# Kernel tuning notes

Measured on AMD Instinct MI355X. Metric: run time of the kernel, lower is better.

## Reference

```python
import jax, jax.numpy as jnp
import numpy as np

B, S, C = 4096, 6, 2048  # batch, num_strips, in_channel
D = C // 8               # query/key projection dim

def setup_inputs() -> dict:
    key = jax.random.key(0)
    k1, k2, k3, k4 = jax.random.split(key, 4)
    sc = 1.0 / np.sqrt(C)
    return {
        "x": jax.random.normal(k1, (B, S, C), dtype=jnp.float32),
        "Wq": jax.random.normal(k2, (D, C), dtype=jnp.float32) * sc,
        "Wk": jax.random.normal(k3, (D, C), dtype=jnp.float32) * sc,
        "Wv": jax.random.normal(k4, (C, C), dtype=jnp.float32) * sc,
        "gamma": jnp.ones((1,), dtype=jnp.float32),
    }

def reference(x, Wq, Wk, Wv, gamma):
    # x: [B, S, C] stacked squeezed strips (feat in the torch code)
    q = jnp.einsum('bsc,dc->bsd', x, Wq)          # [B, S, D]
    k = jnp.einsum('bsc,dc->bsd', x, Wk)          # [B, S, D]
    energy = jnp.einsum('bsd,btd->bst', q, k)     # [B, S, S]
    attention = jax.nn.softmax(energy, axis=-1)   # softmax over keys
    v = jnp.einsum('bsc,dc->bsd', x, Wv)          # [B, S, C]
    out = jnp.einsum('bst,btc->bsc', attention, v)  # [B, S, C]
    out = gamma * out + x                         # gamma-scaled residual
    return out, attention
```

## Files before the change

kernel.cpp:

```cpp
#include <hip/hip_runtime.h>

typedef __attribute__((ext_vector_type(4))) float f32x4;
typedef __attribute__((ext_vector_type(8))) _Float16 f16x8;
typedef __attribute__((ext_vector_type(4))) unsigned short u16x4;
typedef __attribute__((ext_vector_type(8))) unsigned short u16x8;

#define NB 4096
#define NS 6
#define NC 2048
#define MTOT (NB * NS)

static __device__ __forceinline__ unsigned short f2h_bits(float f) {
  _Float16 h = (_Float16)f;
  unsigned short b;
  __builtin_memcpy(&b, &h, 2);
  return b;
}
static __device__ __forceinline__ float h2f(unsigned short b) {
  _Float16 h;
  __builtin_memcpy(&h, &b, 2);
  return (float)h;
}

__global__ void split_x_kernel(const float* __restrict__ x,
                               unsigned short* __restrict__ hi,
                               unsigned short* __restrict__ lo, int n4) {
  int i = blockIdx.x * blockDim.x + threadIdx.x;
  const int stride = gridDim.x * blockDim.x;
  for (; i < n4; i += stride) {
    f32x4 v = reinterpret_cast<const f32x4*>(x)[i];
    u16x4 h, l;
#pragma unroll
    for (int j = 0; j < 4; ++j) {
      const unsigned short hb = f2h_bits(v[j]);
      h[j] = hb;
      l[j] = f2h_bits(v[j] - h2f(hb));
    }
    reinterpret_cast<u16x4*>(hi)[i] = h;
    reinterpret_cast<u16x4*>(lo)[i] = l;
  }
}

__global__ void prep_wqk_kernel(const float* __restrict__ Wq,
                                const float* __restrict__ Wk,
                                unsigned short* __restrict__ w) {
  int i = blockIdx.x * blockDim.x + threadIdx.x;
  const int stride = gridDim.x * blockDim.x;
  for (; i < 262144; i += stride) {
    const int row = i >> 9;
    const int col4 = i & 511;
    const float* src = (row < 256) ? (Wq + (size_t)row * NC)
                                   : (Wk + (size_t)(row - 256) * NC);
    f32x4 v = reinterpret_cast<const f32x4*>(src)[col4];
    u16x4 o;
#pragma unroll
    for (int j = 0; j < 4; ++j) o[j] = f2h_bits(v[j]);
    reinterpret_cast<u16x4*>(w)[i] = o;
  }
}

__global__ void conv_f16_kernel(const float* __restrict__ in,
                                unsigned short* __restrict__ out, int n4) {
  int i = blockIdx.x * blockDim.x + threadIdx.x;
  const int stride = gridDim.x * blockDim.x;
  for (; i < n4; i += stride) {
    f32x4 v = reinterpret_cast<const f32x4*>(in)[i];
    u16x4 o;
#pragma unroll
    for (int j = 0; j < 4; ++j) o[j] = f2h_bits(v[j]);
    reinterpret_cast<u16x4*>(out)[i] = o;
  }
}


#define FENCE() asm volatile("" ::: "memory")
#define BAR() do { FENCE(); __builtin_amdgcn_s_barrier(); FENCE(); } while (0)
#define VM4BAR() do { FENCE(); asm volatile("s_waitcnt vmcnt(4)" ::: "memory"); \
                      __builtin_amdgcn_s_barrier(); FENCE(); } while (0)

template <int MB>
__device__ __forceinline__ void mfma_blk(f32x4 (&acc)[8][4], const f16x8 (&Av)[4],
                                         const f16x8 (&Bv)[4]) {
  __builtin_amdgcn_s_setprio(1);
#pragma unroll
  for (int m = 0; m < 4; ++m)
#pragma unroll
    for (int n = 0; n < 4; ++n)
      acc[MB + m][n] =
          __builtin_amdgcn_mfma_f32_16x16x32_f16(Av[m], Bv[n], acc[MB + m][n], 0, 0, 0);
  __builtin_amdgcn_s_setprio(0);
}

__device__ __forceinline__ void load4(f16x8 (&dst)[4], const char* base, int kk) {
#pragma unroll
  for (int m = 0; m < 4; ++m)
    dst[m] = *reinterpret_cast<const f16x8*>(base + (m * 2 + kk) * 1024);
}

__device__ __forceinline__ void stage_op(const unsigned short* g, int row0, int k0,
                                         char* ldsOp, int wid, int lane) {
  const int sl = lane ^ ((lane >> 4) & 1) ^ (((lane >> 5) & 1) << 1);
#pragma unroll
  for (int h = 0; h < 2; ++h)
#pragma unroll
    for (int i = 0; i < 2; ++i) {
      const int c = wid * 2 + i;
      const unsigned short* src =
          g + (size_t)(row0 + h * 128 + (c >> 1) * 16 + (sl >> 2)) * 2048 +
          (unsigned)(k0 + (c & 1) * 32 + (sl & 3) * 8);
      __builtin_amdgcn_global_load_lds(
          (__attribute__((address_space(1))) void*)src,
          (__attribute__((address_space(3))) void*)(ldsOp + h * 16384 + c * 1024),
          16, 0, 0);
    }
}

template <int NSEG, int N, bool EPI, bool NFAST>
__global__ void __launch_bounds__(512, 2)
gemm256(const unsigned short* __restrict__ A0, const unsigned short* __restrict__ B0,
        const unsigned short* __restrict__ A1, const unsigned short* __restrict__ B1,
        const unsigned short* __restrict__ A2, const unsigned short* __restrict__ B2,
        float* __restrict__ C, const float* __restrict__ resid,
        const float* __restrict__ gam) {
  constexpr int NTPS = 2048 / 64;
  constexpr int NT = NSEG * NTPS;
  constexpr int MT = MTOT / 256;
  constexpr int NXT = N / 256;
  constexpr int NWG = MT * NXT;
  constexpr int CPX = NWG / 8;
  __shared__ char lds[131072];

  const int bid = blockIdx.x;
  const int wg = (bid & 7) * CPX + (bid >> 3);
  const int bx = NFAST ? (wg % NXT) : (wg / MT);
  const int by = NFAST ? (wg / NXT) : (wg % MT);
  const int m0 = by * 256, n0 = bx * 256;

  const int t = threadIdx.x;
  const int lane = t & 63;
  const int wid = t >> 6;
  const int wr = wid >> 2, wc = wid & 3;
  const int laneOff = (lane & 15) * 64 + (lane >> 4) * 16;
  const int swzOff = laneOff ^ (((laneOff >> 9) & 1) << 5) ^ (((laneOff >> 8) & 1) << 4);

  f32x4 acc[8][4] = {};
  f16x8 A03[4], A47[4], Bk0[4], Bk1[4];

  const int aBase = wr * 16384 + swzOff;
  const int bBase = 32768 + (wc >> 1) * 16384 + (wc & 1) * 8192 + swzOff;

#define SEL(P0, P1, P2, S) ((NSEG == 1) ? (P0) : ((S) == 0 ? (P0) : ((S) == 1 ? (P1) : (P2))))
#define WRAPT(TT) ((TT) >= NT ? (TT) - NT : (TT))
#define STAGE_A(TT) do { int tw_ = WRAPT(TT); int s_ = tw_ / NTPS; \
    stage_op(SEL(A0, A1, A2, s_), m0, (tw_ % NTPS) * 64, lds + ((TT) & 1) * 65536, wid, lane); } while (0)
#define STAGE_B(TT) do { int tw_ = WRAPT(TT); int s_ = tw_ / NTPS; \
    stage_op(SEL(B0, B1, B2, s_), n0, (tw_ % NTPS) * 64, lds + ((TT) & 1) * 65536 + 32768, wid, lane); } while (0)

  STAGE_A(0);
  STAGE_B(0);
  STAGE_B(1);
  VM4BAR();

#define TILE(TAU, FIRST) do { \
    char* bufc = lds + ((TAU) & 1) * 65536; \
     \
    load4(A03, bufc + aBase, 0); \
    load4(Bk0, bufc + bBase, 0); \
    STAGE_A((TAU) + 1); \
    BAR(); \
    if (!(FIRST)) mfma_blk<4>(acc, A47, Bk1); \
    BAR(); \
     \
    load4(A47, bufc + aBase + 8192, 0); \
    BAR(); \
    mfma_blk<0>(acc, A03, Bk0); \
    BAR(); \
     \
    load4(A03, bufc + aBase, 1); \
    load4(Bk1, bufc + bBase, 1); \
    BAR(); \
    mfma_blk<4>(acc, A47, Bk0); \
    BAR(); \
     \
    load4(A47, bufc + aBase + 8192, 1); \
    STAGE_B((TAU) + 2); \
    VM4BAR(); \
    mfma_blk<0>(acc, A03, Bk1); \
    BAR(); \
  } while (0)

  TILE(0, 1);
  for (int tau = 1; tau < NT; ++tau) TILE(tau, 0);
  mfma_blk<4>(acc, A47, Bk1);

#undef TILE
#undef STAGE_A
#undef STAGE_B
#undef WRAPT
#undef SEL

  const float g = EPI ? gam[0] : 0.f;
#pragma unroll
  for (int m = 0; m < 8; ++m)
#pragma unroll
    for (int n = 0; n < 4; ++n)
#pragma unroll
      for (int j = 0; j < 4; ++j) {
        const int r = m0 + wr * 128 + m * 16 + (lane >> 4) * 4 + j;
        const int c = n0 + wc * 64 + n * 16 + (lane & 15);
        const size_t idx = (size_t)r * (size_t)N + (size_t)c;
        float v = acc[m][n][j];
        if (EPI) v = g * v + resid[idx];
        C[idx] = v;
      }
}

__global__ void __launch_bounds__(256)
attn_fuse(const float* __restrict__ QK,
          const unsigned short* __restrict__ xh,
          float* __restrict__ attn_out,
          unsigned short* __restrict__ y)
{
  __shared__ float qk[NS * 512];
  __shared__ float eng[36];
  __shared__ float att[36];
  const int b = blockIdx.x;
  const int t = threadIdx.x;
  {
    const f32x4* src = reinterpret_cast<const f32x4*>(QK + (size_t)b * (NS * 512));
    f32x4* dst = reinterpret_cast<f32x4*>(qk);
    for (int i = t; i < (NS * 512) / 4; i += 256) dst[i] = src[i];
  }
  __syncthreads();
  if (t < 144) {
    const int s = t / 24;
    const int rem = t - s * 24;
    const int u = rem >> 2;
    const int sub = rem & 3;
    const float* qr = qk + s * 512;
    const float* kr = qk + u * 512 + 256;
    float sum = 0.f;
    const int d0 = sub * 64;
#pragma unroll 4
    for (int d = 0; d < 64; ++d) sum += qr[d0 + d] * kr[d0 + d];
    sum += __shfl_xor(sum, 1);
    sum += __shfl_xor(sum, 2);
    if (sub == 0) eng[s * 6 + u] = sum;
  }
  __syncthreads();
  if (t < 6) {
    float e[6];
#pragma unroll
    for (int u = 0; u < 6; ++u) e[u] = eng[t * 6 + u];
    float mx = e[0];
#pragma unroll
    for (int u = 1; u < 6; ++u) mx = fmaxf(mx, e[u]);
    float p[6];
    float sm = 0.f;
#pragma unroll
    for (int u = 0; u < 6; ++u) { p[u] = expf(e[u] - mx); sm += p[u]; }
    const float inv = 1.0f / sm;
#pragma unroll
    for (int u = 0; u < 6; ++u) {
      const float a = p[u] * inv;
      att[t * 6 + u] = a;
      attn_out[(size_t)b * 36 + t * 6 + u] = a;
    }
  }
  __syncthreads();
  const unsigned short* xb = xh + (size_t)b * (NS * NC);
  unsigned short* yb = y + (size_t)b * (NS * NC);
  const int c0 = t * 8;
  f32x4 xv[12];
#pragma unroll
  for (int u = 0; u < 6; ++u) {
    u16x8 v = *reinterpret_cast<const u16x8*>(xb + u * NC + c0);
#pragma unroll
    for (int j = 0; j < 4; ++j) {
      xv[2 * u][j] = h2f(v[j]);
      xv[2 * u + 1][j] = h2f(v[4 + j]);
    }
  }
#pragma unroll
  for (int s = 0; s < 6; ++s) {
    f32x4 a0 = 0.f, a1 = 0.f;
#pragma unroll
    for (int u = 0; u < 6; ++u) {
      const float w = att[s * 6 + u];
      a0 += w * xv[2 * u];
      a1 += w * xv[2 * u + 1];
    }
    u16x8 o;
#pragma unroll
    for (int j = 0; j < 4; ++j) { o[j] = f2h_bits(a0[j]); o[4 + j] = f2h_bits(a1[j]); }
    *reinterpret_cast<u16x8*>(yb + s * NC + c0) = o;
  }
}

extern "C" void kernel_launch(void* const* d_in, const int* in_sizes, int n_in,
                              void* d_out, int out_size, void* d_ws, size_t ws_size,
                              hipStream_t stream) {
  (void)in_sizes; (void)n_in; (void)out_size; (void)ws_size;
  const float* x   = (const float*)d_in[0];
  const float* Wq  = (const float*)d_in[1];
  const float* Wk  = (const float*)d_in[2];
  const float* Wv  = (const float*)d_in[3];
  const float* gam = (const float*)d_in[4];
  float* out = (float*)d_out;
  float* attn_out = out + (size_t)MTOT * NC;

  char* ws = (char*)d_ws;
  unsigned short* xh  = (unsigned short*)(ws);
  unsigned short* xl  = (unsigned short*)(ws + 100663296ull);
  unsigned short* wqk = (unsigned short*)(ws + 201326592ull);
  unsigned short* wvh = (unsigned short*)(ws + 203423744ull);
  float*          qkb = (float*)(ws + 211812352ull);

  split_x_kernel<<<2048, 256, 0, stream>>>(x, xh, xl, MTOT * NC / 4);
  prep_wqk_kernel<<<256, 256, 0, stream>>>(Wq, Wk, wqk);
  conv_f16_kernel<<<512, 256, 0, stream>>>(Wv, wvh, NC * NC / 4);

  gemm256<2, 512, false, false><<<192, 512, 0, stream>>>(
      xh, wqk, xl, wqk, nullptr, nullptr, qkb, nullptr, nullptr);

  attn_fuse<<<NB, 256, 0, stream>>>(qkb, xh, attn_out, xl);

  gemm256<1, 2048, true, true><<<768, 512, 0, stream>>>(
      xl, wvh, nullptr, nullptr, nullptr, nullptr, out, x, gam);
}
```

Measured before the change: 491.7 us.

## Split QK GEMM hi/lo K-segments across workgroups and deepen LDS pipeline to 4 stages

The QK projection GEMM no longer loops over both hi and lo halves of x in one workgroup. It launches twice as many workgroups, each handling one segment, and writes two partial results that attn_fuse sums when it loads them. This targets the under-filled 192-workgroup launch on the GPU. The GEMM mainloop also moves from a 2-buffer K=64 tile to a 4-buffer K=32 tile ring with a vmcnt(8) wait, so more global loads are in flight. The cost is an extra partial buffer (held temporarily in the output region), extra reads in attn_fuse, and a change to the schedule of the big V GEMM, which may help or hurt it.

```diff
diff --git a/kernel.cpp b/kernel.cpp
--- a/kernel.cpp
+++ b/kernel.cpp
@@ -75,8 +75,7 @@
 
 #define FENCE() asm volatile("" ::: "memory")
 #define BAR() do { FENCE(); __builtin_amdgcn_s_barrier(); FENCE(); } while (0)
-#define VM4BAR() do { FENCE(); asm volatile("s_waitcnt vmcnt(4)" ::: "memory"); \
-                      __builtin_amdgcn_s_barrier(); FENCE(); } while (0)
+#define VM8() do { FENCE(); asm volatile("s_waitcnt vmcnt(8)" ::: "memory"); } while (0)
 
 template <int MB>
 __device__ __forceinline__ void mfma_blk(f32x4 (&acc)[8][4], const f16x8 (&Av)[4],
@@ -91,50 +90,55 @@
   __builtin_amdgcn_s_setprio(0);
 }
 
-__device__ __forceinline__ void load4(f16x8 (&dst)[4], const char* base, int kk) {
+__device__ __forceinline__ void load4(f16x8 (&dst)[4], const char* base) {
 #pragma unroll
   for (int m = 0; m < 4; ++m)
-    dst[m] = *reinterpret_cast<const f16x8*>(base + (m * 2 + kk) * 1024);
-}
-
-__device__ __forceinline__ void stage_op(const unsigned short* g, int row0, int k0,
-                                         char* ldsOp, int wid, int lane) {
+    dst[m] = *reinterpret_cast<const f16x8*>(base + m * 1024);
+}
+
+__device__ __forceinline__ void stage_tile(const unsigned short* gA,
+                                           const unsigned short* gB, int m0, int n0,
+                                           int k0, char* buf, int wid, int lane) {
   const int sl = lane ^ ((lane >> 4) & 1) ^ (((lane >> 5) & 1) << 1);
-#pragma unroll
-  for (int h = 0; h < 2; ++h)
-#pragma unroll
-    for (int i = 0; i < 2; ++i) {
-      const int c = wid * 2 + i;
-      const unsigned short* src =
-          g + (size_t)(row0 + h * 128 + (c >> 1) * 16 + (sl >> 2)) * 2048 +
-          (unsigned)(k0 + (c & 1) * 32 + (sl & 3) * 8);
-      __builtin_amdgcn_global_load_lds(
-          (__attribute__((address_space(1))) void*)src,
-          (__attribute__((address_space(3))) void*)(ldsOp + h * 16384 + c * 1024),
-          16, 0, 0);
-    }
-}
-
-template <int NSEG, int N, bool EPI, bool NFAST>
+  const int rr = sl >> 2;
+  const int kc = (sl & 3) * 8;
+#pragma unroll
+  for (int i = 0; i < 2; ++i) {
+    const int c = wid * 2 + i;
+    const unsigned short* sA = gA + (size_t)(m0 + c * 16 + rr) * 2048 + (k0 + kc);
+    __builtin_amdgcn_global_load_lds(
+        (__attribute__((address_space(1))) void*)sA,
+        (__attribute__((address_space(3))) void*)(buf + c * 1024), 16, 0, 0);
+    const unsigned short* sB = gB + (size_t)(n0 + c * 16 + rr) * 2048 + (k0 + kc);
+    __builtin_amdgcn_global_load_lds(
+        (__attribute__((address_space(1))) void*)sB,
+        (__attribute__((address_space(3))) void*)(buf + 16384 + c * 1024), 16, 0, 0);
+  }
+}
+
+template <int N, bool EPI, bool NFAST, bool SPLIT>
 __global__ void __launch_bounds__(512, 2)
-gemm256(const unsigned short* __restrict__ A0, const unsigned short* __restrict__ B0,
-        const unsigned short* __restrict__ A1, const unsigned short* __restrict__ B1,
-        const unsigned short* __restrict__ A2, const unsigned short* __restrict__ B2,
-        float* __restrict__ C, const float* __restrict__ resid,
+gemm256(const unsigned short* __restrict__ Ahi, const unsigned short* __restrict__ Alo,
+        const unsigned short* __restrict__ B, float* __restrict__ C0,
+        float* __restrict__ C1, const float* __restrict__ resid,
         const float* __restrict__ gam) {
-  constexpr int NTPS = 2048 / 64;
-  constexpr int NT = NSEG * NTPS;
+  constexpr int NT = 64;
   constexpr int MT = MTOT / 256;
   constexpr int NXT = N / 256;
-  constexpr int NWG = MT * NXT;
+  constexpr int NWGb = MT * NXT;
+  constexpr int NWG = SPLIT ? 2 * NWGb : NWGb;
   constexpr int CPX = NWG / 8;
   __shared__ char lds[131072];
 
   const int bid = blockIdx.x;
   const int wg = (bid & 7) * CPX + (bid >> 3);
-  const int bx = NFAST ? (wg % NXT) : (wg / MT);
-  const int by = NFAST ? (wg / NXT) : (wg % MT);
+  const int seg = SPLIT ? (wg >= NWGb ? 1 : 0) : 0;
+  const int w2 = wg - seg * NWGb;
+  const int bx = NFAST ? (w2 % NXT) : (w2 / MT);
+  const int by = NFAST ? (w2 / NXT) : (w2 % MT);
   const int m0 = by * 256, n0 = bx * 256;
+  const unsigned short* A = seg ? Alo : Ahi;
+  float* C = seg ? C1 : C0;
 
   const int t = threadIdx.x;
   const int lane = t & 63;
@@ -142,62 +146,55 @@
   const int wr = wid >> 2, wc = wid & 3;
   const int laneOff = (lane & 15) * 64 + (lane >> 4) * 16;
   const int swzOff = laneOff ^ (((laneOff >> 9) & 1) << 5) ^ (((laneOff >> 8) & 1) << 4);
+  const int aOff = wr * 8192 + swzOff;
+  const int bOff = 16384 + wc * 4096 + swzOff;
 
   f32x4 acc[8][4] = {};
-  f16x8 A03[4], A47[4], Bk0[4], Bk1[4];
-
-  const int aBase = wr * 16384 + swzOff;
-  const int bBase = 32768 + (wc >> 1) * 16384 + (wc & 1) * 8192 + swzOff;
-
-#define SEL(P0, P1, P2, S) ((NSEG == 1) ? (P0) : ((S) == 0 ? (P0) : ((S) == 1 ? (P1) : (P2))))
+  f16x8 A03[4], A47[4], Be[4], Bo[4];
+
 #define WRAPT(TT) ((TT) >= NT ? (TT) - NT : (TT))
-#define STAGE_A(TT) do { int tw_ = WRAPT(TT); int s_ = tw_ / NTPS; \
-    stage_op(SEL(A0, A1, A2, s_), m0, (tw_ % NTPS) * 64, lds + ((TT) & 1) * 65536, wid, lane); } while (0)
-#define STAGE_B(TT) do { int tw_ = WRAPT(TT); int s_ = tw_ / NTPS; \
-    stage_op(SEL(B0, B1, B2, s_), n0, (tw_ % NTPS) * 64, lds + ((TT) & 1) * 65536 + 32768, wid, lane); } while (0)
-
-  STAGE_A(0);
-  STAGE_B(0);
-  STAGE_B(1);
-  VM4BAR();
-
-#define TILE(TAU, FIRST) do { \
-    char* bufc = lds + ((TAU) & 1) * 65536; \
-     \
-    load4(A03, bufc + aBase, 0); \
-    load4(Bk0, bufc + bBase, 0); \
-    STAGE_A((TAU) + 1); \
+#define STAGE(TT) stage_tile(A, B, m0, n0, WRAPT(TT) * 32, lds + ((TT) & 3) * 32768, wid, lane)
+
+  STAGE(0);
+  STAGE(1);
+  STAGE(2);
+  VM8();
+  BAR();
+
+#define PH0(TAU, BREG, DOMF, BPREV) do { \
+    char* bufc = lds + ((TAU) & 3) * 32768; \
+    load4(A03, bufc + aOff); \
+    load4(BREG, bufc + bOff); \
+    STAGE((TAU) + 3); \
     BAR(); \
-    if (!(FIRST)) mfma_blk<4>(acc, A47, Bk1); \
-    BAR(); \
-     \
-    load4(A47, bufc + aBase + 8192, 0); \
-    BAR(); \
-    mfma_blk<0>(acc, A03, Bk0); \
-    BAR(); \
-     \
-    load4(A03, bufc + aBase, 1); \
-    load4(Bk1, bufc + bBase, 1); \
-    BAR(); \
-    mfma_blk<4>(acc, A47, Bk0); \
-    BAR(); \
-     \
-    load4(A47, bufc + aBase + 8192, 1); \
-    STAGE_B((TAU) + 2); \
-    VM4BAR(); \
-    mfma_blk<0>(acc, A03, Bk1); \
+    if (DOMF) mfma_blk<4>(acc, A47, BPREV); \
     BAR(); \
   } while (0)
-
-  TILE(0, 1);
-  for (int tau = 1; tau < NT; ++tau) TILE(tau, 0);
-  mfma_blk<4>(acc, A47, Bk1);
-
-#undef TILE
-#undef STAGE_A
-#undef STAGE_B
+#define PH1(TAU, BREG) do { \
+    char* bufc = lds + ((TAU) & 3) * 32768; \
+    load4(A47, bufc + aOff + 4096); \
+    VM8(); \
+    BAR(); \
+    mfma_blk<0>(acc, A03, BREG); \
+    BAR(); \
+  } while (0)
+
+  PH0(0, Be, false, Bo);
+  PH1(0, Be);
+  PH0(1, Bo, true, Be);
+  PH1(1, Bo);
+  for (int tau = 2; tau < NT; tau += 2) {
+    PH0(tau, Be, true, Bo);
+    PH1(tau, Be);
+    PH0(tau + 1, Bo, true, Be);
+    PH1(tau + 1, Bo);
+  }
+  mfma_blk<4>(acc, A47, Bo);
+
+#undef PH0
+#undef PH1
+#undef STAGE
 #undef WRAPT
-#undef SEL
 
   const float g = EPI ? gam[0] : 0.f;
 #pragma unroll
@@ -216,7 +213,8 @@
 }
 
 __global__ void __launch_bounds__(256)
-attn_fuse(const float* __restrict__ QK,
+attn_fuse(const float* __restrict__ QK1,
+          const float* __restrict__ QK2,
           const unsigned short* __restrict__ xh,
           float* __restrict__ attn_out,
           unsigned short* __restrict__ y)
@@ -227,9 +225,10 @@
   const int b = blockIdx.x;
   const int t = threadIdx.x;
   {
-    const f32x4* src = reinterpret_cast<const f32x4*>(QK + (size_t)b * (NS * 512));
+    const f32x4* s1 = reinterpret_cast<const f32x4*>(QK1 + (size_t)b * (NS * 512));
+    const f32x4* s2 = reinterpret_cast<const f32x4*>(QK2 + (size_t)b * (NS * 512));
     f32x4* dst = reinterpret_cast<f32x4*>(qk);
-    for (int i = t; i < (NS * 512) / 4; i += 256) dst[i] = src[i];
+    for (int i = t; i < (NS * 512) / 4; i += 256) dst[i] = s1[i] + s2[i];
   }
   __syncthreads();
   if (t < 144) {
@@ -315,16 +314,17 @@
   unsigned short* wqk = (unsigned short*)(ws + 201326592ull);
   unsigned short* wvh = (unsigned short*)(ws + 203423744ull);
   float*          qkb = (float*)(ws + 211812352ull);
+  float*          qk2 = out;
 
   split_x_kernel<<<2048, 256, 0, stream>>>(x, xh, xl, MTOT * NC / 4);
   prep_wqk_kernel<<<256, 256, 0, stream>>>(Wq, Wk, wqk);
   conv_f16_kernel<<<512, 256, 0, stream>>>(Wv, wvh, NC * NC / 4);
 
-  gemm256<2, 512, false, false><<<192, 512, 0, stream>>>(
-      xh, wqk, xl, wqk, nullptr, nullptr, qkb, nullptr, nullptr);
-
-  attn_fuse<<<NB, 256, 0, stream>>>(qkb, xh, attn_out, xl);
-
-  gemm256<1, 2048, true, true><<<768, 512, 0, stream>>>(
-      xl, wvh, nullptr, nullptr, nullptr, nullptr, out, x, gam);
-}
+  gemm256<512, false, false, true><<<384, 512, 0, stream>>>(
+      xh, xl, wqk, qkb, qk2, nullptr, nullptr);
+
+  attn_fuse<<<NB, 256, 0, stream>>>(qkb, qk2, xh, attn_out, xl);
+
+  gemm256<2048, true, true, false><<<768, 512, 0, stream>>>(
+      xl, nullptr, wvh, out, nullptr, x, gam);
+}
```

Result: slower. 550.1 us (+11.9%).
